# Performance work log

Measured on AMD Instinct MI355X. Metric: run time of the kernel, lower is better.

## Reference

```python
import jax, jax.numpy as jnp
import numpy as np

D_MODEL, N_HEADS, D_FF = 1024, 16, 4096
D_HEAD = D_MODEL // N_HEADS
B, S = 2, 2048
EPS = 1e-5


def setup_inputs() -> dict:
    key = jax.random.key(0)
    ks = jax.random.split(key, 12)
    sd = 1.0 / np.sqrt(D_MODEL)
    return {
        "x": jax.random.normal(ks[0], (B, S, D_MODEL), jnp.float32),
        "relative_bias": jax.random.normal(ks[1], (1, N_HEADS, S, S), jnp.float32),
        # attention projections, stored as (in, out) so y = x @ W
        "wq": jax.random.normal(ks[2], (D_MODEL, D_MODEL), jnp.float32) * sd,
        "wk": jax.random.normal(ks[3], (D_MODEL, D_MODEL), jnp.float32) * sd,
        "wv": jax.random.normal(ks[4], (D_MODEL, D_MODEL), jnp.float32) * sd,
        "wo": jax.random.normal(ks[5], (D_MODEL, D_MODEL), jnp.float32) * sd,
        "wo_b": jnp.zeros((D_MODEL,), jnp.float32),
        # FFN
        "w1": jax.random.normal(ks[6], (D_MODEL, D_FF), jnp.float32) * sd,
        "b1": jnp.zeros((D_FF,), jnp.float32),
        "w2": jax.random.normal(ks[7], (D_FF, D_MODEL), jnp.float32) * (1.0 / np.sqrt(D_FF)),
        "b2": jnp.zeros((D_MODEL,), jnp.float32),
        # LayerNorms
        "ln1_g": jnp.ones((D_MODEL,), jnp.float32),
        "ln1_b": jnp.zeros((D_MODEL,), jnp.float32),
        "ln2_g": jnp.ones((D_MODEL,), jnp.float32),
        "ln2_b": jnp.zeros((D_MODEL,), jnp.float32),
    }


def _layernorm(x, g, b):
    mu = jnp.mean(x, axis=-1, keepdims=True)
    var = jnp.mean(jnp.square(x - mu), axis=-1, keepdims=True)
    return (x - mu) * jax.lax.rsqrt(var + EPS) * g + b


def _attn(x, relative_bias, wq, wk, wv, wo, wo_b):
    b, s, d = x.shape
    # (B,S,D) -> (B,H,S,Dh)
    def split_heads(t):
        return t.reshape(b, s, N_HEADS, D_HEAD).transpose(0, 2, 1, 3)
    q = split_heads(x @ wq)
    k = split_heads(x @ wk)
    v = split_heads(x @ wv)
    scores = jnp.einsum("bhqd,bhkd->bhqk", q, k) / np.sqrt(D_HEAD) + relative_bias
    attn = jax.nn.softmax(scores, axis=-1)
    ctx = jnp.einsum("bhqk,bhkd->bhqd", attn, v)
    ctx = ctx.transpose(0, 2, 1, 3).reshape(b, s, d)
    return ctx @ wo + wo_b


def _ffn(x, w1, b1, w2, b2):
    return jax.nn.gelu(x @ w1 + b1, approximate=False) @ w2 + b2


def reference(x, relative_bias, wq, wk, wv, wo, wo_b, w1, b1, w2, b2,
              ln1_g, ln1_b, ln2_g, ln2_b):
    x = x + _attn(_layernorm(x, ln1_g, ln1_b), relative_bias, wq, wk, wv, wo, wo_b)
    x = x + _ffn(_layernorm(x, ln2_g, ln2_b), w1, b1, w2, b2)
    return x
```

## Files before the change

### kernel.cpp

```cpp
#include <hip/hip_runtime.h>
#include <hip/hip_bf16.h>
#include <stdint.h>

typedef unsigned short u16;
typedef __bf16 bf16x8 __attribute__((ext_vector_type(8)));
typedef u16   u16x8  __attribute__((ext_vector_type(8)));
typedef u16   u16x4  __attribute__((ext_vector_type(4)));
typedef u16   u16x2  __attribute__((ext_vector_type(2)));
typedef float f32x4  __attribute__((ext_vector_type(4)));

__device__ __forceinline__ u16 f2bf(float f) {
  union { float f; uint32_t u; } v; v.f = f;
  uint32_t r = v.u + 0x7fffu + ((v.u >> 16) & 1u);
  return (u16)(r >> 16);
}

typedef __attribute__((address_space(1))) void gvoid_t;
typedef __attribute__((address_space(3))) void lvoid_t;
__device__ __forceinline__ void gload_lds16(const void* g, void* l) {
  __builtin_amdgcn_global_load_lds((gvoid_t*)g, (lvoid_t*)l, 16, 0, 0);
}

template<int CTRL>
__device__ __forceinline__ float dpp_f(float x) {
  int i = __builtin_bit_cast(int, x);
  i = __builtin_amdgcn_update_dpp(i, i, CTRL, 0xF, 0xF, true);
  return __builtin_bit_cast(float, i);
}
__device__ __forceinline__ float rowmax16(float x) {
  x = fmaxf(x, dpp_f<0x128>(x));
  x = fmaxf(x, dpp_f<0x124>(x));
  x = fmaxf(x, dpp_f<0x122>(x));
  x = fmaxf(x, dpp_f<0x121>(x));
  return x;
}
__device__ __forceinline__ float rowsum16(float x) {
  x += dpp_f<0x128>(x);
  x += dpp_f<0x124>(x);
  x += dpp_f<0x122>(x);
  x += dpp_f<0x121>(x);
  return x;
}

__global__ __launch_bounds__(256)
void ln_kernel(const float* __restrict__ x, const float* __restrict__ g,
               const float* __restrict__ b, u16* __restrict__ out) {
  const int row = blockIdx.x;
  const int tid = threadIdx.x;
  const float* xr = x + (size_t)row * 1024;
  f32x4 v = *(const f32x4*)&xr[tid * 4];
  float s = v[0] + v[1] + v[2] + v[3];
  float q = v[0]*v[0] + v[1]*v[1] + v[2]*v[2] + v[3]*v[3];
  #pragma unroll
  for (int o = 32; o > 0; o >>= 1) { s += __shfl_xor(s, o); q += __shfl_xor(q, o); }
  __shared__ float ss[4], qq[4];
  if ((tid & 63) == 0) { ss[tid >> 6] = s; qq[tid >> 6] = q; }
  __syncthreads();
  s = ss[0] + ss[1] + ss[2] + ss[3];
  q = qq[0] + qq[1] + qq[2] + qq[3];
  float mu = s * (1.0f / 1024.0f);
  float var = q * (1.0f / 1024.0f) - mu * mu;
  float rstd = rsqrtf(var + 1e-5f);
  u16x4 o4;
  #pragma unroll
  for (int i = 0; i < 4; ++i)
    o4[i] = f2bf((v[i] - mu) * rstd * g[tid * 4 + i] + b[tid * 4 + i]);
  *(u16x4*)&out[(size_t)row * 1024 + tid * 4] = o4;
}

__global__ __launch_bounds__(256)
void transpose_cast(const float* __restrict__ W, u16* __restrict__ Wt, int K, int N) {
  __shared__ float t[32][33];
  const int n0 = blockIdx.x * 32, k0 = blockIdx.y * 32;
  const int tx = threadIdx.x & 31, ty = threadIdx.x >> 5;
  #pragma unroll
  for (int i = 0; i < 4; ++i)
    t[ty + 8*i][tx] = W[(size_t)(k0 + ty + 8*i) * N + n0 + tx];
  __syncthreads();
  #pragma unroll
  for (int i = 0; i < 4; ++i)
    Wt[(size_t)(n0 + ty + 8*i) * K + k0 + tx] = f2bf(t[tx][ty + 8*i]);
}

template<int EPI>
__global__ __launch_bounds__(256, 2)
void gemm_bt(const u16* __restrict__ A, const u16* __restrict__ Bt,
             void* __restrict__ out, const float* __restrict__ bias,
             const float* __restrict__ resid, int M, int N, int K) {
  __shared__ u16 As[128 * 32];
  __shared__ u16 Bs[128 * 32];
  const int tid = threadIdx.x;
  const int w = tid >> 6, l = tid & 63;
  const int bm = blockIdx.x * 128, bn = blockIdx.y * 128;
  const int wr = (w >> 1) * 64, wc = (w & 1) * 64;
  const int l15 = l & 15, lhi = l >> 4;
  f32x4 acc[4][4] = {};

  const int r4 = tid >> 2;
  const int c8 = (tid & 3) * 8;
  const u16* ga0 = A  + (size_t)(bm + r4) * K + c8;
  const u16* ga1 = ga0 + (size_t)64 * K;
  const u16* gb0 = Bt + (size_t)(bn + r4) * K + c8;
  const u16* gb1 = gb0 + (size_t)64 * K;
  u16* lA0 = &As[(w * 16) * 32];
  u16* lA1 = &As[(64 + w * 16) * 32];
  u16* lB0 = &Bs[(w * 16) * 32];
  u16* lB1 = &Bs[(64 + w * 16) * 32];

  const int arow = (wr + l15) * 32 + lhi * 8;
  const int brow = (wc + l15) * 32 + lhi * 8;

  for (int k0 = 0; k0 < K; k0 += 32) {
    gload_lds16(ga0 + k0, lA0);
    gload_lds16(ga1 + k0, lA1);
    gload_lds16(gb0 + k0, lB0);
    gload_lds16(gb1 + k0, lB1);
    __syncthreads();
    bf16x8 a[4], b[4];
    #pragma unroll
    for (int m = 0; m < 4; ++m) a[m] = *(const bf16x8*)&As[arow + m * 16 * 32];
    #pragma unroll
    for (int n = 0; n < 4; ++n) b[n] = *(const bf16x8*)&Bs[brow + n * 16 * 32];
    #pragma unroll
    for (int m = 0; m < 4; ++m)
      #pragma unroll
      for (int n = 0; n < 4; ++n)
        acc[m][n] = __builtin_amdgcn_mfma_f32_16x16x32_bf16(a[m], b[n], acc[m][n], 0, 0, 0);
    __syncthreads();
  }

  #pragma unroll
  for (int m = 0; m < 4; ++m) {
    #pragma unroll
    for (int n = 0; n < 4; ++n) {
      #pragma unroll
      for (int r = 0; r < 4; ++r) {
        const int grow = bm + wr + m * 16 + lhi * 4 + r;
        const int gcol = bn + wc + n * 16 + l15;
        float vv = acc[m][n][r];
        if constexpr (EPI >= 1) vv += bias[gcol];
        if constexpr (EPI == 1) vv = 0.5f * vv * (1.0f + erff(vv * 0.70710678118f));
        if constexpr (EPI == 2) {
          vv += resid[(size_t)grow * N + gcol];
          ((float*)out)[(size_t)grow * N + gcol] = vv;
        } else {
          ((u16*)out)[(size_t)grow * N + gcol] = f2bf(vv);
        }
      }
    }
  }
}

template<int EPI>
__global__ __launch_bounds__(256, 2)
void gemm_bt64(const u16* __restrict__ A, const u16* __restrict__ Bt,
               void* __restrict__ out, const float* __restrict__ bias,
               const float* __restrict__ resid, int M, int N, int K) {
  __shared__ u16 As[64 * 32];
  __shared__ u16 Bs[128 * 32];
  const int tid = threadIdx.x;
  const int w = tid >> 6, l = tid & 63;
  const int bm = blockIdx.x * 64, bn = blockIdx.y * 128;
  const int wr = (w & 1) * 32, wc = (w >> 1) * 64;
  const int l15 = l & 15, lhi = l >> 4;
  f32x4 acc[2][4] = {};

  const int r4 = tid >> 2;
  const int c8 = (tid & 3) * 8;
  const u16* ga0 = A  + (size_t)(bm + r4) * K + c8;
  const u16* gb0 = Bt + (size_t)(bn + r4) * K + c8;
  const u16* gb1 = gb0 + (size_t)64 * K;
  u16* lA0 = &As[(w * 16) * 32];
  u16* lB0 = &Bs[(w * 16) * 32];
  u16* lB1 = &Bs[(64 + w * 16) * 32];

  const int arow = (wr + l15) * 32 + lhi * 8;
  const int brow = (wc + l15) * 32 + lhi * 8;

  for (int k0 = 0; k0 < K; k0 += 32) {
    gload_lds16(ga0 + k0, lA0);
    gload_lds16(gb0 + k0, lB0);
    gload_lds16(gb1 + k0, lB1);
    __syncthreads();
    bf16x8 a[2], b[4];
    #pragma unroll
    for (int m = 0; m < 2; ++m) a[m] = *(const bf16x8*)&As[arow + m * 16 * 32];
    #pragma unroll
    for (int n = 0; n < 4; ++n) b[n] = *(const bf16x8*)&Bs[brow + n * 16 * 32];
    #pragma unroll
    for (int m = 0; m < 2; ++m)
      #pragma unroll
      for (int n = 0; n < 4; ++n)
        acc[m][n] = __builtin_amdgcn_mfma_f32_16x16x32_bf16(a[m], b[n], acc[m][n], 0, 0, 0);
    __syncthreads();
  }

  #pragma unroll
  for (int m = 0; m < 2; ++m) {
    #pragma unroll
    for (int n = 0; n < 4; ++n) {
      #pragma unroll
      for (int r = 0; r < 4; ++r) {
        const int grow = bm + wr + m * 16 + lhi * 4 + r;
        const int gcol = bn + wc + n * 16 + l15;
        float vv = acc[m][n][r];
        if constexpr (EPI >= 1) vv += bias[gcol];
        if constexpr (EPI == 1) vv = 0.5f * vv * (1.0f + erff(vv * 0.70710678118f));
        if constexpr (EPI == 2) {
          vv += resid[(size_t)grow * N + gcol];
          ((float*)out)[(size_t)grow * N + gcol] = vv;
        } else {
          ((u16*)out)[(size_t)grow * N + gcol] = f2bf(vv);
        }
      }
    }
  }
}

#define SWZ(row) ((((row) & 7) ^ (((row) >> 3) & 7)) << 3)

__global__ __launch_bounds__(256)
void attn_kernel(const u16* __restrict__ qkv, const float* __restrict__ bias,
                 u16* __restrict__ ctx) {
  const int qt = blockIdx.x;
  const int bh = blockIdx.y;
  const int b = bh >> 4, h = bh & 15;
  const int tid = threadIdx.x, w = tid >> 6, l = tid & 63;
  const int l15 = l & 15, lhi = l >> 4;
  const size_t ld = 3072;
  const float L2E = 1.44269504f;

  __shared__ u16 Kl[2][4096];
  __shared__ u16 Vt[2][4096];
  __shared__ u16 Pl[4][1024];

  const u16* qp = qkv;
  const u16* kp = qkv + 1024;
  const u16* vp = qkv + 2048;

  const int key2 = (tid >> 3) * 2, dg8 = (tid & 7) * 8;
  const u16* kbase = kp + ((size_t)b * 2048 + key2) * ld + h * 64 + dg8;
  const u16* vbase = vp + ((size_t)b * 2048 + key2) * ld + h * 64 + dg8;

  bf16x8 qf0, qf1;
  {
    const u16* qrow = qp + ((size_t)b * 2048 + qt * 64 + w * 16 + l15) * ld + h * 64 + lhi * 8;
    qf0 = *(const bf16x8*)qrow;
    qf1 = *(const bf16x8*)(qrow + 32);
  }

  const float* bg0 = bias + ((size_t)h * 2048 + qt * 64 + w * 16 + lhi * 4) * 2048 + l15;
  const float* bp0 = bg0;
  const float* bp1 = bg0 + 2048;
  const float* bp2 = bg0 + 4096;
  const float* bp3 = bg0 + 6144;

  float m_run[4], s_run[4];
  f32x4 octx[4] = {};
  #pragma unroll
  for (int r = 0; r < 4; ++r) { m_run[r] = -1e30f; s_run[r] = 0.f; }

  u16x8 kpf[2], vpf[2];
  float bfA[16], bfB[16];

  auto load_kv = [&](int kv) {
    kpf[0] = *(const u16x8*)(kbase + (size_t)kv * ld);
    kpf[1] = *(const u16x8*)(kbase + (size_t)(kv + 1) * ld);
    vpf[0] = *(const u16x8*)(vbase + (size_t)kv * ld);
    vpf[1] = *(const u16x8*)(vbase + (size_t)(kv + 1) * ld);
  };
  auto load_bias = [&](float (&bf)[16]) {
    bf[0]  = bp0[0];  bf[1]  = bp0[16]; bf[2]  = bp0[32]; bf[3]  = bp0[48];
    bf[4]  = bp1[0];  bf[5]  = bp1[16]; bf[6]  = bp1[32]; bf[7]  = bp1[48];
    bf[8]  = bp2[0];  bf[9]  = bp2[16]; bf[10] = bp2[32]; bf[11] = bp2[48];
    bf[12] = bp3[0];  bf[13] = bp3[16]; bf[14] = bp3[32]; bf[15] = bp3[48];
    bp0 += 64; bp1 += 64; bp2 += 64; bp3 += 64;
  };
  auto store_kv = [&](u16* Kd, u16* Vd) {
    *(u16x8*)&Kd[(key2)     * 64 + (dg8 ^ SWZ(key2))]     = kpf[0];
    *(u16x8*)&Kd[(key2 + 1) * 64 + (dg8 ^ SWZ(key2 + 1))] = kpf[1];
    #pragma unroll
    for (int i = 0; i < 8; ++i) {
      const int d = dg8 + i;
      u16x2 vq = { vpf[0][i], vpf[1][i] };
      *(u16x2*)&Vd[d * 64 + (key2 ^ SWZ(d))] = vq;
    }
  };

  load_kv(0);
  load_bias(bfA);
  load_bias(bfB);
  store_kv(Kl[0], Vt[0]);
  load_kv(64);
  __syncthreads();

  auto iter = [&](int it, int cur, float (&bc)[16]) {
    if (it < 31) store_kv(Kl[cur ^ 1], Vt[cur ^ 1]);
    if (it < 30) load_kv((it + 2) * 64);

    f32x4 sa[4] = {};
    #pragma unroll
    for (int nf = 0; nf < 4; ++nf) {
      const int row = nf * 16 + l15;
      const int s = SWZ(row);
      bf16x8 kf0 = *(const bf16x8*)&Kl[cur][row * 64 + ((lhi * 8) ^ s)];
      bf16x8 kf1 = *(const bf16x8*)&Kl[cur][row * 64 + ((32 + lhi * 8) ^ s)];
      sa[nf] = __builtin_amdgcn_mfma_f32_16x16x32_bf16(qf0, kf0, sa[nf], 0, 0, 0);
      sa[nf] = __builtin_amdgcn_mfma_f32_16x16x32_bf16(qf1, kf1, sa[nf], 0, 0, 0);
    }

    float p[4][4];
    #pragma unroll
    for (int r = 0; r < 4; ++r)
      #pragma unroll
      for (int nf = 0; nf < 4; ++nf)
        p[r][nf] = fmaf(sa[nf][r], 0.125f, bc[r * 4 + nf]);
    if (it < 30) load_bias(bc);

    #pragma unroll
    for (int r = 0; r < 4; ++r) {
      float mx = fmaxf(fmaxf(p[r][0], p[r][1]), fmaxf(p[r][2], p[r][3]));
      mx = rowmax16(mx);
      if (mx > m_run[r] + 5.545177f) {
        const float fs = exp2f((m_run[r] - mx) * L2E);
        s_run[r] *= fs;
        #pragma unroll
        for (int nf = 0; nf < 4; ++nf) octx[nf][r] *= fs;
        m_run[r] = mx;
      }
      const float nml = -m_run[r] * L2E;
      float e0 = exp2f(fmaf(p[r][0], L2E, nml));
      float e1 = exp2f(fmaf(p[r][1], L2E, nml));
      float e2 = exp2f(fmaf(p[r][2], L2E, nml));
      float e3 = exp2f(fmaf(p[r][3], L2E, nml));
      p[r][0] = e0; p[r][1] = e1; p[r][2] = e2; p[r][3] = e3;
      s_run[r] += rowsum16((e0 + e1) + (e2 + e3));
    }

    #pragma unroll
    for (int r = 0; r < 4; ++r) {
      const int row = lhi * 4 + r;
      const int s = SWZ(row);
      #pragma unroll
      for (int nf = 0; nf < 4; ++nf)
        Pl[w][row * 64 + ((nf * 16 + l15) ^ s)] =
            __builtin_bit_cast(u16, (__bf16)p[r][nf]);
    }

    #pragma unroll
    for (int ks = 0; ks < 2; ++ks) {
      bf16x8 pa = *(const bf16x8*)&Pl[w][l15 * 64 + ((ks * 32 + lhi * 8) ^ SWZ(l15))];
      #pragma unroll
      for (int nf = 0; nf < 4; ++nf) {
        const int row = nf * 16 + l15;
        bf16x8 bv = *(const bf16x8*)&Vt[cur][row * 64 + ((ks * 32 + lhi * 8) ^ SWZ(row))];
        octx[nf] = __builtin_amdgcn_mfma_f32_16x16x32_bf16(pa, bv, octx[nf], 0, 0, 0);
      }
    }

    __syncthreads();
  };

  for (int i2 = 0; i2 < 16; ++i2) {
    iter(2 * i2,     0, bfA);
    iter(2 * i2 + 1, 1, bfB);
  }

  float inv[4];
  #pragma unroll
  for (int r = 0; r < 4; ++r) inv[r] = 1.0f / s_run[r];
  #pragma unroll
  for (int nf = 0; nf < 4; ++nf)
    #pragma unroll
    for (int r = 0; r < 4; ++r) {
      const int grow = b * 2048 + qt * 64 + w * 16 + lhi * 4 + r;
      const int gcol = h * 64 + nf * 16 + l15;
      ctx[(size_t)grow * 1024 + gcol] = f2bf(octx[nf][r] * inv[r]);
    }
}

extern "C" void kernel_launch(void* const* d_in, const int* in_sizes, int n_in,
                              void* d_out, int out_size, void* d_ws, size_t ws_size,
                              hipStream_t stream) {
  const float* x    = (const float*)d_in[0];
  const float* rb   = (const float*)d_in[1];
  const float* wq   = (const float*)d_in[2];
  const float* wk   = (const float*)d_in[3];
  const float* wv   = (const float*)d_in[4];
  const float* wo   = (const float*)d_in[5];
  const float* wo_b = (const float*)d_in[6];
  const float* w1   = (const float*)d_in[7];
  const float* b1   = (const float*)d_in[8];
  const float* w2   = (const float*)d_in[9];
  const float* b2   = (const float*)d_in[10];
  const float* ln1g = (const float*)d_in[11];
  const float* ln1b = (const float*)d_in[12];
  const float* ln2g = (const float*)d_in[13];
  const float* ln2b = (const float*)d_in[14];

  char* ws = (char*)d_ws;
  u16*   xn    = (u16*)(ws + 0);
  u16*   qkvb  = (u16*)(ws + (8u << 20));
  u16*   hbuf  = (u16*)(ws + (8u << 20));
  u16*   ctxb  = (u16*)(ws + (32u << 20));
  float* x1    = (float*)(ws + (40u << 20));
  u16*   wqkvt = (u16*)(ws + (56u << 20));
  u16*   wot   = (u16*)(ws + (62u << 20));
  u16*   w1t   = (u16*)(ws + (64u << 20));
  u16*   w2t   = (u16*)(ws + (72u << 20));

  transpose_cast<<<dim3(32, 32),  256, 0, stream>>>(wq, wqkvt,               1024, 1024);
  transpose_cast<<<dim3(32, 32),  256, 0, stream>>>(wk, wqkvt + 1024 * 1024, 1024, 1024);
  transpose_cast<<<dim3(32, 32),  256, 0, stream>>>(wv, wqkvt + 2048 * 1024, 1024, 1024);
  transpose_cast<<<dim3(32, 32),  256, 0, stream>>>(wo, wot,                 1024, 1024);
  transpose_cast<<<dim3(128, 32), 256, 0, stream>>>(w1, w1t,                 1024, 4096);
  transpose_cast<<<dim3(32, 128), 256, 0, stream>>>(w2, w2t,                 4096, 1024);

  ln_kernel<<<4096, 256, 0, stream>>>(x, ln1g, ln1b, xn);
  gemm_bt<0><<<dim3(32, 24), 256, 0, stream>>>(xn, wqkvt, qkvb, nullptr, nullptr, 4096, 3072, 1024);
  attn_kernel<<<dim3(32, 32), 256, 0, stream>>>(qkvb, rb, ctxb);
  gemm_bt64<2><<<dim3(64, 8), 256, 0, stream>>>(ctxb, wot, x1, wo_b, x, 4096, 1024, 1024);
  ln_kernel<<<4096, 256, 0, stream>>>(x1, ln2g, ln2b, xn);
  gemm_bt<1><<<dim3(32, 32), 256, 0, stream>>>(xn, w1t, hbuf, b1, nullptr, 4096, 4096, 1024);
  gemm_bt64<2><<<dim3(64, 8), 256, 0, stream>>>(hbuf, w2t, (float*)d_out, b2, x1, 4096, 1024, 4096);

  (void)in_sizes; (void)n_in; (void)out_size; (void)ws_size;
}
```

Measured before the change: 404.8 us.

## Double-buffer GEMM LDS tiles with async prefetch and lighter barriers

Both bf16 GEMM kernels now keep two LDS buffers, issue the global-to-LDS loads for the next K step before computing the current one, and wait only on the older loads with explicit vmcnt waits plus raw s_barrier. This is meant to hide global load latency behind MFMA work instead of stalling at each step. The attention kernel swaps __syncthreads for a barrier that waits only on LDS counters, so its outstanding global prefetches are not drained at each iteration. The cost is doubled LDS use in the GEMMs, which may reduce occupancy, and correctness now depends on the hand-written waitcnt logic.

```diff
diff --git a/kernel.cpp b/kernel.cpp
--- a/kernel.cpp
+++ b/kernel.cpp
@@ -19,6 +19,16 @@
 typedef __attribute__((address_space(3))) void lvoid_t;
 __device__ __forceinline__ void gload_lds16(const void* g, void* l) {
   __builtin_amdgcn_global_load_lds((gvoid_t*)g, (lvoid_t*)l, 16, 0, 0);
+}
+
+__device__ __forceinline__ void barrier_lgkm() {
+  asm volatile("s_waitcnt lgkmcnt(0)\ns_barrier" ::: "memory");
+}
+__device__ __forceinline__ void bar_only() {
+  asm volatile("s_barrier" ::: "memory");
+}
+template<int N> __device__ __forceinline__ void wait_vm() {
+  asm volatile("s_waitcnt vmcnt(%0)" :: "n"(N) : "memory");
 }
 
 template<int CTRL>
@@ -87,8 +97,8 @@
 void gemm_bt(const u16* __restrict__ A, const u16* __restrict__ Bt,
              void* __restrict__ out, const float* __restrict__ bias,
              const float* __restrict__ resid, int M, int N, int K) {
-  __shared__ u16 As[128 * 32];
-  __shared__ u16 Bs[128 * 32];
+  __shared__ u16 As[2][128 * 32];
+  __shared__ u16 Bs[2][128 * 32];
   const int tid = threadIdx.x;
   const int w = tid >> 6, l = tid & 63;
   const int bm = blockIdx.x * 128, bn = blockIdx.y * 128;
@@ -102,31 +112,35 @@
   const u16* ga1 = ga0 + (size_t)64 * K;
   const u16* gb0 = Bt + (size_t)(bn + r4) * K + c8;
   const u16* gb1 = gb0 + (size_t)64 * K;
-  u16* lA0 = &As[(w * 16) * 32];
-  u16* lA1 = &As[(64 + w * 16) * 32];
-  u16* lB0 = &Bs[(w * 16) * 32];
-  u16* lB1 = &Bs[(64 + w * 16) * 32];
 
   const int arow = (wr + l15) * 32 + lhi * 8;
   const int brow = (wc + l15) * 32 + lhi * 8;
 
-  for (int k0 = 0; k0 < K; k0 += 32) {
-    gload_lds16(ga0 + k0, lA0);
-    gload_lds16(ga1 + k0, lA1);
-    gload_lds16(gb0 + k0, lB0);
-    gload_lds16(gb1 + k0, lB1);
-    __syncthreads();
+  auto stage = [&](int k0, int buf) {
+    gload_lds16(ga0 + k0, &As[buf][(w * 16) * 32]);
+    gload_lds16(ga1 + k0, &As[buf][(64 + w * 16) * 32]);
+    gload_lds16(gb0 + k0, &Bs[buf][(w * 16) * 32]);
+    gload_lds16(gb1 + k0, &Bs[buf][(64 + w * 16) * 32]);
+  };
+
+  const int nsteps = K >> 5;
+  stage(0, 0);
+  for (int s = 0; s < nsteps; ++s) {
+    const int cur = s & 1;
+    if (s + 1 < nsteps) { stage((s + 1) << 5, cur ^ 1); wait_vm<4>(); }
+    else                { wait_vm<0>(); }
+    bar_only();
     bf16x8 a[4], b[4];
     #pragma unroll
-    for (int m = 0; m < 4; ++m) a[m] = *(const bf16x8*)&As[arow + m * 16 * 32];
-    #pragma unroll
-    for (int n = 0; n < 4; ++n) b[n] = *(const bf16x8*)&Bs[brow + n * 16 * 32];
+    for (int m = 0; m < 4; ++m) a[m] = *(const bf16x8*)&As[cur][arow + m * 16 * 32];
+    #pragma unroll
+    for (int n = 0; n < 4; ++n) b[n] = *(const bf16x8*)&Bs[cur][brow + n * 16 * 32];
     #pragma unroll
     for (int m = 0; m < 4; ++m)
       #pragma unroll
       for (int n = 0; n < 4; ++n)
         acc[m][n] = __builtin_amdgcn_mfma_f32_16x16x32_bf16(a[m], b[n], acc[m][n], 0, 0, 0);
-    __syncthreads();
+    bar_only();
   }
 
   #pragma unroll
@@ -156,8 +170,8 @@
 void gemm_bt64(const u16* __restrict__ A, const u16* __restrict__ Bt,
                void* __restrict__ out, const float* __restrict__ bias,
                const float* __restrict__ resid, int M, int N, int K) {
-  __shared__ u16 As[64 * 32];
-  __shared__ u16 Bs[128 * 32];
+  __shared__ u16 As[2][64 * 32];
+  __shared__ u16 Bs[2][128 * 32];
   const int tid = threadIdx.x;
   const int w = tid >> 6, l = tid & 63;
   const int bm = blockIdx.x * 64, bn = blockIdx.y * 128;
@@ -170,29 +184,34 @@
   const u16* ga0 = A  + (size_t)(bm + r4) * K + c8;
   const u16* gb0 = Bt + (size_t)(bn + r4) * K + c8;
   const u16* gb1 = gb0 + (size_t)64 * K;
-  u16* lA0 = &As[(w * 16) * 32];
-  u16* lB0 = &Bs[(w * 16) * 32];
-  u16* lB1 = &Bs[(64 + w * 16) * 32];
 
   const int arow = (wr + l15) * 32 + lhi * 8;
   const int brow = (wc + l15) * 32 + lhi * 8;
 
-  for (int k0 = 0; k0 < K; k0 += 32) {
-    gload_lds16(ga0 + k0, lA0);
-    gload_lds16(gb0 + k0, lB0);
-    gload_lds16(gb1 + k0, lB1);
-    __syncthreads();
+  auto stage = [&](int k0, int buf) {
+    gload_lds16(ga0 + k0, &As[buf][(w * 16) * 32]);
+    gload_lds16(gb0 + k0, &Bs[buf][(w * 16) * 32]);
+    gload_lds16(gb1 + k0, &Bs[buf][(64 + w * 16) * 32]);
+  };
+
+  const int nsteps = K >> 5;
+  stage(0, 0);
+  for (int s = 0; s < nsteps; ++s) {
+    const int cur = s & 1;
+    if (s + 1 < nsteps) { stage((s + 1) << 5, cur ^ 1); wait_vm<3>(); }
+    else                { wait_vm<0>(); }
+    bar_only();
     bf16x8 a[2], b[4];
     #pragma unroll
-    for (int m = 0; m < 2; ++m) a[m] = *(const bf16x8*)&As[arow + m * 16 * 32];
-    #pragma unroll
-    for (int n = 0; n < 4; ++n) b[n] = *(const bf16x8*)&Bs[brow + n * 16 * 32];
+    for (int m = 0; m < 2; ++m) a[m] = *(const bf16x8*)&As[cur][arow + m * 16 * 32];
+    #pragma unroll
+    for (int n = 0; n < 4; ++n) b[n] = *(const bf16x8*)&Bs[cur][brow + n * 16 * 32];
     #pragma unroll
     for (int m = 0; m < 2; ++m)
       #pragma unroll
       for (int n = 0; n < 4; ++n)
         acc[m][n] = __builtin_amdgcn_mfma_f32_16x16x32_bf16(a[m], b[n], acc[m][n], 0, 0, 0);
-    __syncthreads();
+    bar_only();
   }
 
   #pragma unroll
@@ -292,7 +311,7 @@
   load_bias(bfB);
   store_kv(Kl[0], Vt[0]);
   load_kv(64);
-  __syncthreads();
+  barrier_lgkm();
 
   auto iter = [&](int it, int cur, float (&bc)[16]) {
     if (it < 31) store_kv(Kl[cur ^ 1], Vt[cur ^ 1]);
@@ -358,7 +377,7 @@
       }
     }
 
-    __syncthreads();
+    barrier_lgkm();
   };
 
   for (int i2 = 0; i2 < 16; ++i2) {
```

Measured after the change: 390.6 us. -3.5%, faster.
